# Kernel optimization log

Hardware: AMD Instinct MI355X
Metric: run time of the kernel (lower is better)

The kernel has to match this reference:

```python
import jax, jax.numpy as jnp
import numpy as np

THRESH = 0.3
OUT_THRESH = 0.3
LENS = 0.5  # surrogate-gradient window (ActFun in snn-delays repo)


@jax.custom_vjp
def spike(x):
    # Heaviside spike with rectangular surrogate gradient
    return (x > 0.0).astype(x.dtype)

def _spike_fwd(x):
    return spike(x), x

def _spike_bwd(x, g):
    return (g * (jnp.abs(x) < LENS).astype(g.dtype),)

spike.defvjp(_spike_fwd, _spike_bwd)


def setup_inputs() -> dict:
    key = jax.random.key(0)
    ks = jax.random.split(key, 7)
    B, T, I, H, O = 256, 50, 1024, 2048, 20
    # binary input spikes (rate ~0.2), as an SNN would receive
    inp = (jax.random.uniform(ks[0], (B, T, I)) < 0.2).astype(jnp.float32)
    # Linear(in, out, bias=False) -> weight [out, in], Kaiming-uniform-ish init
    w_ih = jax.random.uniform(ks[1], (H, I), minval=-1.0, maxval=1.0) / np.sqrt(I)
    w_hh = jax.random.uniform(ks[2], (H, H), minval=-1.0, maxval=1.0) / np.sqrt(H)
    w_ho = jax.random.uniform(ks[3], (O, H), minval=-1.0, maxval=1.0) / np.sqrt(H)
    tau_m_h = 0.83 + 0.1 * jax.random.normal(ks[4], (H,))
    tau_m_o = 0.83 + 0.1 * jax.random.normal(ks[5], (O,))
    return {"input": inp, "w_ih": w_ih, "w_hh": w_hh, "w_ho": w_ho,
            "tau_m_h": tau_m_h, "tau_m_o": tau_m_o}


def _rsnn_forward(inp, w_ih, w_hh, w_ho, tau_m_h, tau_m_o):
    B, T, I = inp.shape
    H = w_ih.shape[0]
    O = w_ho.shape[0]
    alpha_h = jnp.exp(-1.0 / tau_m_h)  # [H]
    alpha_o = jnp.exp(-1.0 / tau_m_o)  # [O]
    zH = jnp.zeros((B, H), inp.dtype)
    zO = jnp.zeros((B, O), inp.dtype)

    def step(carry, x_t):
        h_mem, h_spk, o_mem, o_spk, o_sum, mot = carry
        # hidden membrane update: input + recurrent + decayed (reset-gated) mem
        h_mem = (x_t @ w_ih.T) + (h_spk @ w_hh.T) + h_mem * alpha_h * (1.0 - h_spk)
        h_spk = spike(h_mem - THRESH)
        # output membrane update
        o_mem = o_mem * alpha_o * (1.0 - o_spk) + h_spk @ w_ho.T
        o_spk = spike(o_mem - OUT_THRESH)
        o_sum = o_sum + o_spk
        mot = mot + jax.nn.softmax(o_mem, axis=1)
        return (h_mem, h_spk, o_mem, o_spk, o_sum, mot), None

    init = (zH, zH, zO, zO, zO, zO)
    (h_mem, h_spk, o_mem, o_spk, o_sum, mot), _ = jax.lax.scan(
        step, init, jnp.swapaxes(inp, 0, 1))  # scan over time [T,B,I]
    return o_sum / T, mot


def reference(input, w_ih, w_hh, w_ho, tau_m_h, tau_m_o):
    return _rsnn_forward(input, w_ih, w_hh, w_ho, tau_m_h, tau_m_o)
```

## Files before the change

kernel.cpp:

```cpp
#include <hip/hip_runtime.h>
#include <stdint.h>
#include <math.h>


#define B_   256
#define T_   50
#define I_   1024
#define H_   2048
#define O_   20
#define XIN_T  262144
#define XS_BUF 524288
#define WNT 294912
#define WPL 98304

typedef __attribute__((ext_vector_type(4))) int intx4;
typedef long long ll_t;

__device__ __forceinline__ int digit_of(float v, int p) {
  int W = (int)rintf(v * 134217728.0f);
  int c0 = ((W + 128) & 255) - 128;
  int W1 = (W - c0) >> 8;
  int c1 = ((W1 + 128) & 255) - 128;
  int W2 = (W1 - c1) >> 8;
  return (p == 0) ? c0 : (p == 1) ? c1 : W2;
}

__global__ void prep_w(const float* __restrict__ w_ih,
                       const float* __restrict__ w_hh,
                       int8_t* __restrict__ Wtl) {
  int blk = blockIdx.x;
  int n = blk / 9, kg = blk % 9;
  int k9 = (kg * 256 + (int)threadIdx.x) * 4;
  int p = k9 / 3072, kk = k9 % 3072;
  const float* src = (kk < 1024) ? (w_ih + n * I_ + kk)
                                 : (w_hh + n * H_ + (kk - 1024));
  float4 v = *(const float4*)src;
  int d0 = digit_of(v.x, p) & 255;
  int d1 = digit_of(v.y, p) & 255;
  int d2 = digit_of(v.z, p) & 255;
  int d3 = digit_of(v.w, p) & 255;
  int packed = d0 | (d1 << 8) | (d2 << 16) | (d3 << 24);
  size_t off = (size_t)(n >> 5) * WNT + (size_t)p * WPL + (kk >> 6) * 2048 +
               (n & 31) * 64 + (kk & 63);
  *(int*)(Wtl + off) = packed;
}

__global__ void init_k(int8_t* __restrict__ Xin, int8_t* __restrict__ Xs,
                       float* __restrict__ Hm, const float* __restrict__ input,
                       const float* __restrict__ tau_h,
                       const float* __restrict__ tau_o,
                       float* __restrict__ AlphaH, float* __restrict__ AlphaO,
                       const float* __restrict__ w_ho, double* __restrict__ WhoD,
                       float* __restrict__ Om, float* __restrict__ Osp,
                       float* __restrict__ Osu, float* __restrict__ Mo) {
  int id = blockIdx.x * 256 + threadIdx.x;
  {
    int b = id >> 8, i4 = (id & 255) * 4;
    for (int t = 0; t < T_; ++t) {
      float4 v = *(const float4*)(input + ((size_t)(b * T_ + t) << 10) + i4);
      uchar4 pk;
      pk.x = v.x > 0.5f ? 1 : 0;
      pk.y = v.y > 0.5f ? 1 : 0;
      pk.z = v.z > 0.5f ? 1 : 0;
      pk.w = v.w > 0.5f ? 1 : 0;
      *(uchar4*)(Xin + (size_t)t * XIN_T + (b >> 6) * 65536 + (i4 >> 6) * 4096 +
                 (b & 63) * 64 + (i4 & 63)) = pk;
    }
  }
  *(double*)(Xs + (size_t)id * 8) = 0.0;
  *(float4*)(Hm + (size_t)id * 8) = make_float4(0.f, 0.f, 0.f, 0.f);
  *(float4*)(Hm + (size_t)id * 8 + 4) = make_float4(0.f, 0.f, 0.f, 0.f);
  if (id < 64 * O_ * 32) {
    int nt = id / 640, rem = id % 640, o = rem / 32, hl = rem & 31;
    WhoD[id] = (double)w_ho[o * H_ + nt * 32 + hl];
  }
  if (id < H_) AlphaH[id] = (float)exp((double)(-1.0f / tau_h[id]));
  if (id < O_) AlphaO[id] = (float)exp((double)(-1.0f / tau_o[id]));
  if (id < B_ * O_) {
    Om[id] = 0.f; Osp[id] = 0.f; Osu[id] = 0.f; Mo[id] = 0.f;
  }
}

__global__ __launch_bounds__(512, 2) void step_k(
    const int8_t* __restrict__ Wtl, const int8_t* __restrict__ Xin,
    int8_t* __restrict__ Xs, float* __restrict__ Hm, double* __restrict__ Po,
    const double* __restrict__ WhoD, const float* __restrict__ AlphaH,
    const float* __restrict__ AlphaO, float* __restrict__ Om,
    float* __restrict__ Osp, float* __restrict__ Osu, float* __restrict__ Mo,
    int t) {
  __shared__ double WhoL[640];
  __shared__ __align__(16) int8_t red[98304];
  __shared__ int8_t spk_lT[2048];

  const int j = blockIdx.x;
  const int nt = (j & 7) * 8 + ((j >> 3) & 7);
  const int mg = j >> 6;
  const int tid = threadIdx.x;
  const int l = tid & 63, k = tid >> 6;
  const int r_ = l & 15, q = l >> 4;
  const int kb = k & 1, kq = k >> 1;

  for (int i = tid; i < 640; i += 512) WhoL[i] = WhoD[nt * 640 + i];

  const int fr_e = kq >> 1;
  const int fc_e = kq & 1;
  const int h_e = nt * 32 + fc_e * 16 + r_;

  const int u0 = kq * 12;
  const int8_t* Bw = Wtl + (size_t)nt * WNT + r_ * 64 + q * 16;
  const int arow = r_ * 64 + q * 16;

#define REDP(w, idx) (red + (((w) * 12 + (idx)) * 64 + l) * 16)

  const int8_t* Ain = Xin + (size_t)t * XIN_T + mg * 65536 + kb * 2048 + arow;
  const int8_t* Asp =
      Xs + (size_t)(t & 1) * XS_BUF + mg * 131072 + kb * 2048 + arow;
  int8_t* Xw = Xs + (size_t)((t + 1) & 1) * XS_BUF;

  intx4 acc[2][2][3];
#pragma unroll
  for (int fr = 0; fr < 2; ++fr)
#pragma unroll
    for (int fc = 0; fc < 2; ++fc)
#pragma unroll
      for (int p = 0; p < 3; ++p) acc[fr][fc][p] = (intx4){0, 0, 0, 0};

  intx4 a[2][2], b[2][2][3];
  {
    const int8_t* ap = (u0 < 16) ? (Ain + u0 * 4096) : (Asp + (u0 - 16) * 4096);
    a[0][0] = *(const intx4*)ap;
    a[0][1] = *(const intx4*)(ap + 1024);
    const int8_t* bp = Bw + (size_t)u0 * 2048;
#pragma unroll
    for (int p = 0; p < 3; ++p)
#pragma unroll
      for (int fc = 0; fc < 2; ++fc)
        b[0][fc][p] = *(const intx4*)(bp + p * WPL + fc * 1024);
  }
#pragma unroll
  for (int i = 0; i < 12; ++i) {
    const int cur = i & 1, nxt = cur ^ 1;
    if (i < 11) {
      const int un = u0 + i + 1;
      const int8_t* ap =
          (un < 16) ? (Ain + un * 4096) : (Asp + (un - 16) * 4096);
      a[nxt][0] = *(const intx4*)ap;
      a[nxt][1] = *(const intx4*)(ap + 1024);
      const int8_t* bp = Bw + (size_t)un * 2048;
#pragma unroll
      for (int p = 0; p < 3; ++p)
#pragma unroll
        for (int fc = 0; fc < 2; ++fc)
          b[nxt][fc][p] = *(const intx4*)(bp + p * WPL + fc * 1024);
    }
#pragma unroll
    for (int p = 0; p < 3; ++p)
#pragma unroll
      for (int fc = 0; fc < 2; ++fc) {
        acc[0][fc][p] = __builtin_amdgcn_mfma_i32_16x16x64_i8(
            a[cur][0], b[cur][fc][p], acc[0][fc][p], 0, 0, 0);
        acc[1][fc][p] = __builtin_amdgcn_mfma_i32_16x16x64_i8(
            a[cur][1], b[cur][fc][p], acc[1][fc][p], 0, 0, 0);
      }
  }

#pragma unroll
  for (int fr = 0; fr < 2; ++fr)
#pragma unroll
    for (int fc = 0; fc < 2; ++fc)
#pragma unroll
      for (int p = 0; p < 3; ++p)
        *(intx4*)REDP(k, (fr * 2 + fc) * 3 + p) = acc[fr][fc][p];
  __syncthreads();
  {
    const int base = (fr_e * 2 + fc_e) * 3;
    intx4 s0 = (intx4){0, 0, 0, 0}, s1 = s0, s2 = s0;
#pragma unroll
    for (int w = 0; w < 4; ++w) {
      const int wi = w * 2 + kb;
      s0 = s0 + *(const intx4*)REDP(wi, base + 0);
      s1 = s1 + *(const intx4*)REDP(wi, base + 1);
      s2 = s2 + *(const intx4*)REDP(wi, base + 2);
    }
    const float alpha = AlphaH[h_e];
    unsigned spkpack = 0;
#pragma unroll
    for (int jj = 0; jj < 4; ++jj) {
      ll_t Sv = (ll_t)s0[jj] + ((ll_t)s1[jj] << 8) + ((ll_t)s2[jj] << 16);
      float M = (float)((double)Sv * 7.450580596923828125e-9);
      const int brl = kb * 32 + fr_e * 16 + q * 4 + jj;
      const int idx = (mg * 64 + brl) * H_ + h_e;
      float hp = Hm[idx];
      float spf = (hp - 0.3f) > 0.f ? 1.f : 0.f;
      float hmn = M + hp * alpha * (1.0f - spf);
      Hm[idx] = hmn;
      unsigned spk = (hmn - 0.3f) > 0.f ? 1u : 0u;
      Xw[mg * 131072 + (h_e >> 6) * 4096 + brl * 64 + (h_e & 63)] =
          (int8_t)spk;
      spkpack |= spk << (8 * jj);
    }
    *(unsigned*)(spk_lT + (fc_e * 16 + r_) * 64 + kb * 32 + fr_e * 16 +
                 q * 4) = spkpack;
  }
  __syncthreads();

  if (tid < 256) {
    const int bl = tid >> 2, og = (tid & 3) * 5;
    const double* W0 = WhoL + og * 32;
    double a0 = 0, a1 = 0, a2 = 0, a3 = 0, a4 = 0;
#pragma unroll
    for (int hl = 0; hl < 32; ++hl) {
      double m = (double)spk_lT[hl * 64 + bl];
      a0 += m * W0[hl];
      a1 += m * W0[32 + hl];
      a2 += m * W0[64 + hl];
      a3 += m * W0[96 + hl];
      a4 += m * W0[128 + hl];
    }
    double* dst =
        Po + ((size_t)((t & 1) * 256 + mg * 64 + bl) * 64 + nt) * 20 + og;
    dst[0] = a0; dst[1] = a1; dst[2] = a2; dst[3] = a3; dst[4] = a4;
  } else if (k == 7 && t > 0) {
    float m = -3.0e38f;
    if (l < O_) {
      const double* pp = Po + ((size_t)(((t - 1) & 1) * 256 + j) * 64) * 20 + l;
      double s = 0.0;
#pragma unroll
      for (int n2 = 0; n2 < 64; ++n2) s += pp[n2 * 20];
      m = Om[j * O_ + l] * AlphaO[l] * (1.0f - Osp[j * O_ + l]) + (float)s;
    }
    float mx = m;
#pragma unroll
    for (int off = 16; off > 0; off >>= 1)
      mx = fmaxf(mx, __shfl_xor(mx, off, 32));
    float eo = (l < O_) ? expf(m - mx) : 0.f;
    float se = eo;
#pragma unroll
    for (int off = 16; off > 0; off >>= 1) se += __shfl_xor(se, off, 32);
    if (l < O_) {
      float sp = (m - 0.3f) > 0.f ? 1.f : 0.f;
      Om[j * O_ + l] = m;
      Osp[j * O_ + l] = sp;
      Osu[j * O_ + l] += sp;
      Mo[j * O_ + l] += eo / se;
    }
  }
#undef REDP
}

__global__ void final_k(const double* __restrict__ Po,
                        const float* __restrict__ AlphaO,
                        const float* __restrict__ Om,
                        const float* __restrict__ Osp,
                        const float* __restrict__ Osu,
                        const float* __restrict__ Mo, float* __restrict__ out) {
  __shared__ float om_l[O_];
  const int j = blockIdx.x, tid = threadIdx.x;
  if (tid < O_) {
    const double* pp = Po + ((size_t)(256 + j) * 64) * 20 + tid;
    double s = 0.0;
#pragma unroll
    for (int n2 = 0; n2 < 64; ++n2) s += pp[n2 * 20];
    float r = (float)s;
    float m = Om[j * O_ + tid] * AlphaO[tid] * (1.0f - Osp[j * O_ + tid]) + r;
    om_l[tid] = m;
  }
  __syncthreads();
  if (tid < O_) {
    float m = om_l[tid];
    float mx = om_l[0];
#pragma unroll
    for (int o = 1; o < O_; ++o) mx = fmaxf(mx, om_l[o]);
    float se = 0.f;
#pragma unroll
    for (int o = 0; o < O_; ++o) se += expf(om_l[o] - mx);
    float sp = (m - 0.3f) > 0.f ? 1.f : 0.f;
    out[j * O_ + tid] = (Osu[j * O_ + tid] + sp) / 50.0f;
    out[B_ * O_ + j * O_ + tid] = Mo[j * O_ + tid] + expf(m - mx) / se;
  }
}

extern "C" void kernel_launch(void* const* d_in, const int* in_sizes, int n_in,
                              void* d_out, int out_size, void* d_ws, size_t ws_size,
                              hipStream_t stream) {
  const float* input = (const float*)d_in[0];
  const float* w_ih  = (const float*)d_in[1];
  const float* w_hh  = (const float*)d_in[2];
  const float* w_ho  = (const float*)d_in[3];
  const float* tau_h = (const float*)d_in[4];
  const float* tau_o = (const float*)d_in[5];

  char* ws = (char*)d_ws;
  int8_t* Wtl    = (int8_t*)(ws);
  int8_t* Xin    = (int8_t*)(ws + 18874368);
  int8_t* Xs     = (int8_t*)(ws + 31981568);
  double* Po     = (double*)(ws + 33030144);
  float*  Hm     = (float*)(ws + 38273024);
  double* WhoD   = (double*)(ws + 40370176);
  float*  AlphaH = (float*)(ws + 40697856);
  float*  AlphaO = (float*)(ws + 40706048);
  float*  Om     = (float*)(ws + 40706176);
  float*  Osp    = (float*)(ws + 40726656);
  float*  Osu    = (float*)(ws + 40747136);
  float*  Mo     = (float*)(ws + 40767616);
  float*  out    = (float*)d_out;

  prep_w<<<2048 * 9, 256, 0, stream>>>(w_ih, w_hh, Wtl);
  init_k<<<256, 256, 0, stream>>>(Xin, Xs, Hm, input, tau_h, tau_o, AlphaH,
                                  AlphaO, w_ho, WhoD, Om, Osp, Osu, Mo);
  for (int t = 0; t < T_; ++t) {
    step_k<<<256, 512, 0, stream>>>(Wtl, Xin, Xs, Hm, Po, WhoD, AlphaH, AlphaO,
                                    Om, Osp, Osu, Mo, t);
  }
  final_k<<<256, 64, 0, stream>>>(Po, AlphaO, Om, Osp, Osu, Mo, out);
}
```

Baseline: 1.036 ms.

## Remap warp MFMA tiles to 4x1 fragments and transpose hidden-membrane layout

Each warp now computes four row fragments against a single column fragment instead of a 2x2 fragment block. This cuts B-weight register loads per K step and changes how the cross-warp split-K reduction is indexed. The hidden membrane state is stored hidden-major so each lane reads and writes four batch values with one float4 access instead of four scalar accesses. The trade-off is more A-operand loads per step and a strided Hm access pattern across lanes.

```diff
diff --git a/kernel.cpp b/kernel.cpp
--- a/kernel.cpp
+++ b/kernel.cpp
@@ -98,44 +98,39 @@
   const int tid = threadIdx.x;
   const int l = tid & 63, k = tid >> 6;
   const int r_ = l & 15, q = l >> 4;
-  const int kb = k & 1, kq = k >> 1;
+  const int fcg = k >> 2, kq = k & 3;
 
   for (int i = tid; i < 640; i += 512) WhoL[i] = WhoD[nt * 640 + i];
 
-  const int fr_e = kq >> 1;
-  const int fc_e = kq & 1;
+  const int fr_e = k & 3;
+  const int fc_e = k >> 2;
   const int h_e = nt * 32 + fc_e * 16 + r_;
 
   const int u0 = kq * 12;
-  const int8_t* Bw = Wtl + (size_t)nt * WNT + r_ * 64 + q * 16;
+  const int8_t* Bw =
+      Wtl + (size_t)nt * WNT + fcg * 1024 + r_ * 64 + q * 16;
   const int arow = r_ * 64 + q * 16;
 
 #define REDP(w, idx) (red + (((w) * 12 + (idx)) * 64 + l) * 16)
 
-  const int8_t* Ain = Xin + (size_t)t * XIN_T + mg * 65536 + kb * 2048 + arow;
-  const int8_t* Asp =
-      Xs + (size_t)(t & 1) * XS_BUF + mg * 131072 + kb * 2048 + arow;
+  const int8_t* Ain = Xin + (size_t)t * XIN_T + mg * 65536 + arow;
+  const int8_t* Asp = Xs + (size_t)(t & 1) * XS_BUF + mg * 131072 + arow;
   int8_t* Xw = Xs + (size_t)((t + 1) & 1) * XS_BUF;
 
-  intx4 acc[2][2][3];
-#pragma unroll
-  for (int fr = 0; fr < 2; ++fr)
-#pragma unroll
-    for (int fc = 0; fc < 2; ++fc)
-#pragma unroll
-      for (int p = 0; p < 3; ++p) acc[fr][fc][p] = (intx4){0, 0, 0, 0};
-
-  intx4 a[2][2], b[2][2][3];
+  intx4 acc[4][3];
+#pragma unroll
+  for (int fr = 0; fr < 4; ++fr)
+#pragma unroll
+    for (int p = 0; p < 3; ++p) acc[fr][p] = (intx4){0, 0, 0, 0};
+
+  intx4 a[2][4], b[2][3];
   {
     const int8_t* ap = (u0 < 16) ? (Ain + u0 * 4096) : (Asp + (u0 - 16) * 4096);
-    a[0][0] = *(const intx4*)ap;
-    a[0][1] = *(const intx4*)(ap + 1024);
+#pragma unroll
+    for (int fr = 0; fr < 4; ++fr) a[0][fr] = *(const intx4*)(ap + fr * 1024);
     const int8_t* bp = Bw + (size_t)u0 * 2048;
 #pragma unroll
-    for (int p = 0; p < 3; ++p)
-#pragma unroll
-      for (int fc = 0; fc < 2; ++fc)
-        b[0][fc][p] = *(const intx4*)(bp + p * WPL + fc * 1024);
+    for (int p = 0; p < 3; ++p) b[0][p] = *(const intx4*)(bp + p * WPL);
   }
 #pragma unroll
   for (int i = 0; i < 12; ++i) {
@@ -144,63 +139,58 @@
       const int un = u0 + i + 1;
       const int8_t* ap =
           (un < 16) ? (Ain + un * 4096) : (Asp + (un - 16) * 4096);
-      a[nxt][0] = *(const intx4*)ap;
-      a[nxt][1] = *(const intx4*)(ap + 1024);
+#pragma unroll
+      for (int fr = 0; fr < 4; ++fr) a[nxt][fr] = *(const intx4*)(ap + fr * 1024);
       const int8_t* bp = Bw + (size_t)un * 2048;
 #pragma unroll
-      for (int p = 0; p < 3; ++p)
-#pragma unroll
-        for (int fc = 0; fc < 2; ++fc)
-          b[nxt][fc][p] = *(const intx4*)(bp + p * WPL + fc * 1024);
+      for (int p = 0; p < 3; ++p) b[nxt][p] = *(const intx4*)(bp + p * WPL);
     }
 #pragma unroll
     for (int p = 0; p < 3; ++p)
 #pragma unroll
-      for (int fc = 0; fc < 2; ++fc) {
-        acc[0][fc][p] = __builtin_amdgcn_mfma_i32_16x16x64_i8(
-            a[cur][0], b[cur][fc][p], acc[0][fc][p], 0, 0, 0);
-        acc[1][fc][p] = __builtin_amdgcn_mfma_i32_16x16x64_i8(
-            a[cur][1], b[cur][fc][p], acc[1][fc][p], 0, 0, 0);
-      }
-  }
-
-#pragma unroll
-  for (int fr = 0; fr < 2; ++fr)
-#pragma unroll
-    for (int fc = 0; fc < 2; ++fc)
-#pragma unroll
-      for (int p = 0; p < 3; ++p)
-        *(intx4*)REDP(k, (fr * 2 + fc) * 3 + p) = acc[fr][fc][p];
+      for (int fr = 0; fr < 4; ++fr)
+        acc[fr][p] = __builtin_amdgcn_mfma_i32_16x16x64_i8(
+            a[cur][fr], b[cur][p], acc[fr][p], 0, 0, 0);
+  }
+
+#pragma unroll
+  for (int fr = 0; fr < 4; ++fr)
+#pragma unroll
+    for (int p = 0; p < 3; ++p)
+      *(intx4*)REDP(k, fr * 3 + p) = acc[fr][p];
   __syncthreads();
   {
-    const int base = (fr_e * 2 + fc_e) * 3;
+    const int base = fr_e * 3;
     intx4 s0 = (intx4){0, 0, 0, 0}, s1 = s0, s2 = s0;
 #pragma unroll
     for (int w = 0; w < 4; ++w) {
-      const int wi = w * 2 + kb;
+      const int wi = fc_e * 4 + w;
       s0 = s0 + *(const intx4*)REDP(wi, base + 0);
       s1 = s1 + *(const intx4*)REDP(wi, base + 1);
       s2 = s2 + *(const intx4*)REDP(wi, base + 2);
     }
     const float alpha = AlphaH[h_e];
+    float* hp_ptr = Hm + h_e * 256 + mg * 64 + fr_e * 16 + q * 4;
+    float4 hp4 = *(float4*)hp_ptr;
+    float* hp = reinterpret_cast<float*>(&hp4);
     unsigned spkpack = 0;
 #pragma unroll
     for (int jj = 0; jj < 4; ++jj) {
       ll_t Sv = (ll_t)s0[jj] + ((ll_t)s1[jj] << 8) + ((ll_t)s2[jj] << 16);
       float M = (float)((double)Sv * 7.450580596923828125e-9);
-      const int brl = kb * 32 + fr_e * 16 + q * 4 + jj;
-      const int idx = (mg * 64 + brl) * H_ + h_e;
-      float hp = Hm[idx];
-      float spf = (hp - 0.3f) > 0.f ? 1.f : 0.f;
-      float hmn = M + hp * alpha * (1.0f - spf);
-      Hm[idx] = hmn;
+      float hpv = hp[jj];
+      float spf = (hpv - 0.3f) > 0.f ? 1.f : 0.f;
+      float hmn = M + hpv * alpha * (1.0f - spf);
+      hp[jj] = hmn;
       unsigned spk = (hmn - 0.3f) > 0.f ? 1u : 0u;
+      const int brl = fr_e * 16 + q * 4 + jj;
       Xw[mg * 131072 + (h_e >> 6) * 4096 + brl * 64 + (h_e & 63)] =
           (int8_t)spk;
       spkpack |= spk << (8 * jj);
     }
-    *(unsigned*)(spk_lT + (fc_e * 16 + r_) * 64 + kb * 32 + fr_e * 16 +
-                 q * 4) = spkpack;
+    *(float4*)hp_ptr = hp4;
+    *(unsigned*)(spk_lT + (fc_e * 16 + r_) * 64 + fr_e * 16 + q * 4) =
+        spkpack;
   }
   __syncthreads();
 
```

New measurement: 971.8 us. -6.2%, faster.
